# Kernel optimization log

Hardware: AMD Instinct MI355X
Metric: run time of the kernel (lower is better)

Reference implementation:

```python
import jax, jax.numpy as jnp
import numpy as np

B, T, DIM, DZ = 512, 256, 128, 256
H = 2 * DZ  # LSTM hidden size (per direction)
RESIDUAL = False


def _lstm_cell(xt, h, c, Wih, Whh, bih, bhh):
    # PyTorch gate order: input, forget, cell, output
    g = xt @ Wih.T + bih + h @ Whh.T + bhh
    i, f, gg, o = jnp.split(g, 4, axis=-1)
    c2 = jax.nn.sigmoid(f) * c + jax.nn.sigmoid(i) * jnp.tanh(gg)
    h2 = jax.nn.sigmoid(o) * jnp.tanh(c2)
    return h2, c2


def _masked_lstm(xs, lengths, Wih, Whh, bih, bhh):
    # Packed-sequence semantics: state frozen and output zero past each length.
    Bn, Tn, _ = xs.shape
    Hn = Whh.shape[1]

    def step(carry, inp):
        h, c = carry
        xt, t = inp
        h2, c2 = _lstm_cell(xt, h, c, Wih, Whh, bih, bhh)
        m = (t < lengths)[:, None]
        h = jnp.where(m, h2, h)
        c = jnp.where(m, c2, c)
        return (h, c), jnp.where(m, h2, 0.0)

    init = (jnp.zeros((Bn, Hn), xs.dtype), jnp.zeros((Bn, Hn), xs.dtype))
    _, hs = jax.lax.scan(step, init, (xs.swapaxes(0, 1), jnp.arange(Tn)))
    return hs.swapaxes(0, 1)  # [B,T,H]


def setup_inputs() -> dict:
    key = jax.random.key(0)
    ks = jax.random.split(key, 24)
    rn = lambda k, *s: jax.random.normal(k, s, jnp.float32) * 0.02
    z = jnp.zeros
    return {
        "x": jax.random.normal(ks[0], (B, T, DIM), jnp.float32),
        "x_lengths": jax.random.randint(ks[1], (B,), 1, T + 1),
        "norm_g": jnp.ones((T, DIM)), "norm_b": z((T, DIM)),
        "We": rn(ks[2], DZ, DIM), "be": z((DZ,)),
        "Wih_f": rn(ks[3], 4 * H, DZ), "Whh_f": rn(ks[4], 4 * H, H),
        "bih_f": z((4 * H,)), "bhh_f": z((4 * H,)),
        "Wih_b": rn(ks[5], 4 * H, DZ), "Whh_b": rn(ks[6], 4 * H, H),
        "bih_b": z((4 * H,)), "bhh_b": z((4 * H,)),
        "W1e": rn(ks[7], H, 2 * H), "b1e": z((H,)),
        "W2e": rn(ks[8], DZ, H), "b2e": z((DZ,)),
        "Wd": rn(ks[9], DZ, DZ), "bd": z((DZ,)),
        "Wp1": rn(ks[10], DZ, DZ), "bp1": z((DZ,)),
        "Wp2": rn(ks[11], DIM, DZ), "bp2": z((DIM,)),
        "Wih_d": rn(ks[12], 4 * H, DZ + DIM), "Whh_d": rn(ks[13], 4 * H, H),
        "bih_d": z((4 * H,)), "bhh_d": z((4 * H,)),
        "W1d": rn(ks[14], DZ, H), "b1d": z((DZ,)),
        "W2d": rn(ks[15], DIM, DZ), "b2d": z((DIM,)),
    }


def _forward(x, x_lengths, norm_g, norm_b, We, be,
             Wih_f, Whh_f, bih_f, bhh_f, Wih_b, Whh_b, bih_b, bhh_b,
             W1e, b1e, W2e, b2e,
             Wd, bd, Wp1, bp1, Wp2, bp2,
             Wih_d, Whh_d, bih_d, bhh_d, W1d, b1d, W2d, b2d):
    # ----- encoder -----
    # LayerNorm over the last two dims [T, DIM] per sample
    mu = x.mean(axis=(1, 2), keepdims=True)
    var = x.var(axis=(1, 2), keepdims=True)
    xn = (x - mu) / jnp.sqrt(var + 1e-5) * norm_g + norm_b
    xe = jax.nn.relu(xn @ We.T + be)  # [B,T,DZ]

    hs_f = _masked_lstm(xe, x_lengths, Wih_f, Whh_f, bih_f, bhh_f)
    # backward direction: reverse each valid prefix, run, scatter back
    rev_idx = jnp.clip(x_lengths[:, None] - 1 - jnp.arange(T)[None, :], 0)  # [B,T]
    xe_rev = jnp.take_along_axis(xe, rev_idx[:, :, None], axis=1)
    hs_b_rev = _masked_lstm(xe_rev, x_lengths, Wih_b, Whh_b, bih_b, bhh_b)
    hs_b = jnp.take_along_axis(hs_b_rev, rev_idx[:, :, None], axis=1)
    valid = (jnp.arange(T)[None, :] < x_lengths[:, None])[:, :, None]
    out = jnp.concatenate([hs_f, jnp.where(valid, hs_b, 0.0)], axis=-1)  # [B,T,2H]
    out = out.sum(axis=1) / x_lengths[:, None].astype(x.dtype)
    out = jax.nn.relu(out @ W1e.T + b1e)
    zlat = out @ W2e.T + b2e  # [B,DZ]

    x0 = jax.nn.relu(zlat @ Wd.T + bd)
    pose0 = jax.nn.relu(x0 @ Wp1.T + bp1) @ Wp2.T + bp2  # [B,DIM]
    h0 = jnp.zeros((x.shape[0], H), x.dtype)

    def dstep(carry, _):
        h, c, pose = carry
        inp = jnp.concatenate([x0, pose], axis=1)
        h2, c2 = _lstm_cell(inp, h, c, Wih_d, Whh_d, bih_d, bhh_d)
        h_ = jax.nn.relu(h2 @ W1d.T + b1d)
        new_pose = h_ @ W2d.T + b2d
        if RESIDUAL:
            new_pose = new_pose + pose
        return (h2, c2, new_pose), new_pose

    _, poses = jax.lax.scan(dstep, (h0, h0, pose0), None, length=T)
    return poses.swapaxes(0, 1)  # [B,T,DIM]


def reference(x, x_lengths, norm_g, norm_b, We, be,
              Wih_f, Whh_f, bih_f, bhh_f, Wih_b, Whh_b, bih_b, bhh_b,
              W1e, b1e, W2e, b2e,
              Wd, bd, Wp1, bp1, Wp2, bp2,
              Wih_d, Whh_d, bih_d, bhh_d, W1d, b1d, W2d, b2d):
    dec = _forward(x, x_lengths, norm_g, norm_b, We, be,
                   Wih_f, Whh_f, bih_f, bhh_f, Wih_b, Whh_b, bih_b, bhh_b,
                   W1e, b1e, W2e, b2e,
                   Wd, bd, Wp1, bp1, Wp2, bp2,
                   Wih_d, Whh_d, bih_d, bhh_d, W1d, b1d, W2d, b2d)
    return (x, dec, x_lengths)
```

## Files before the change

kernel.cpp:

```cpp
#include <hip/hip_runtime.h>
#include <stdint.h>
#include <math.h>

typedef unsigned short u16;
typedef unsigned char u8;
typedef unsigned u32;
typedef unsigned long long u64;
typedef short s16x8 __attribute__((ext_vector_type(8)));
typedef int i32x2 __attribute__((ext_vector_type(2)));
typedef __bf16 bv8 __attribute__((ext_vector_type(8)));
typedef float f32x4 __attribute__((ext_vector_type(4)));

#define DEV static __device__ __forceinline__

DEV float b2f(u16 x){ union{unsigned u; float f;} v; v.u=((unsigned)x)<<16; return v.f; }
DEV u16 f2b(float f){ union{float f; unsigned u;} v; v.f=f; unsigned u=v.u; u += 0x7fff + ((u>>16)&1u); return (u16)(u>>16); }
DEV float sigm(float x){ return 1.f/(1.f+__expf(-x)); }
DEV float tanh_(float x){ float cx=fminf(fmaxf(x,-20.f),20.f); float e=__expf(2.f*cx); return (e-1.f)/(e+1.f); }
DEV f32x4 mfma16(bv8 a, bv8 b, f32x4 c){ return __builtin_amdgcn_mfma_f32_16x16x32_bf16(a,b,c,0,0,0); }
DEV f32x4 mfma8(u64 a, u64 b, f32x4 c){ return __builtin_amdgcn_mfma_f32_16x16x32_fp8_fp8((long)a,(long)b,c,0,0,0); }
DEV bv8 ldf(const u16* p){ return __builtin_bit_cast(bv8, *(const s16x8*)p); }
DEV u8 f2e4(float f){ return (u8)__builtin_amdgcn_cvt_pk_fp8_f32(f, f, 0, false); }

DEV unsigned ald4(const unsigned* p){ return __hip_atomic_load(p, __ATOMIC_RELAXED, __HIP_MEMORY_SCOPE_AGENT); }

DEV void gld8(u64& d, const u8* p){
  asm volatile("global_load_dwordx2 %0, %1, off sc0 sc1" : "=&v"(d) : "v"(p));
}
DEV void gldc8(u64& d, const u8* p){
  asm volatile("global_load_dwordx2 %0, %1, off" : "=&v"(d) : "v"(p));
}
DEV void gst4(u8* p, u32 v){
  asm volatile("global_store_dword %0, %1, off sc0 sc1" :: "v"(p), "v"(v) : "memory");
}
template<int N> DEV void wvm(){
  asm volatile("s_waitcnt vmcnt(%0)" :: "i"(N) : "memory");
  __builtin_amdgcn_sched_barrier(0);
}

DEV void arrive(unsigned* flags, int my, unsigned e){
  asm volatile("s_waitcnt vmcnt(0)" ::: "memory");
  __syncthreads();
  if (threadIdx.x==0)
    __hip_atomic_store(&flags[my*32], e, __ATOMIC_RELAXED, __HIP_MEMORY_SCOPE_AGENT);
}
DEV void waitflags(unsigned* flags, int lo, int n, unsigned e){
  int t = (int)threadIdx.x;
  if (t>=lo && t<lo+n){
    unsigned v;
    do {
      asm volatile("global_load_dword %0, %1, off sc0 sc1\ns_waitcnt vmcnt(0)" : "=&v"(v) : "v"(flags + t*32) : "memory");
      if (v>=e) break;
      __builtin_amdgcn_s_sleep(1);
    } while (1);
  }
  __syncthreads();
}

struct CvtJobs { const float* s[14]; u16* d[14]; int start[14]; };

__global__ __launch_bounds__(256) void cvt_w(CvtJobs J){
  int blk = blockIdx.x, tid = threadIdx.x;
  int j = 0;
  #pragma unroll
  for (int k=1;k<14;k++) if (blk >= J.start[k]) j = k;
  size_t idx = (size_t)(blk - J.start[j])*2048 + (size_t)tid*8;
  const f32x4* ps = (const f32x4*)(J.s[j] + idx);
  f32x4 a = ps[0], b = ps[1];
  s16x8 o;
  #pragma unroll
  for (int i=0;i<4;i++){ o[i]=(short)f2b(a[i]); o[4+i]=(short)f2b(b[i]); }
  *(s16x8*)(J.d[j] + idx) = o;
}

struct Cvt8Jobs { const float* s[7]; u8* d[7]; int start[7]; };

__global__ __launch_bounds__(256) void cvt_w8(Cvt8Jobs J){
  int blk = blockIdx.x, tid = threadIdx.x;
  int j = 0;
  #pragma unroll
  for (int k=1;k<7;k++) if (blk >= J.start[k]) j = k;
  size_t idx = (size_t)(blk - J.start[j])*2048 + (size_t)tid*8;
  const f32x4* ps = (const f32x4*)(J.s[j] + idx);
  f32x4 a = ps[0], b = ps[1];
  int w0 = __builtin_amdgcn_cvt_pk_fp8_f32(a[0]*64.f, a[1]*64.f, 0, false);
  w0 = __builtin_amdgcn_cvt_pk_fp8_f32(a[2]*64.f, a[3]*64.f, w0, true);
  int w1 = __builtin_amdgcn_cvt_pk_fp8_f32(b[0]*64.f, b[1]*64.f, 0, false);
  w1 = __builtin_amdgcn_cvt_pk_fp8_f32(b[2]*64.f, b[3]*64.f, w1, true);
  i32x2 o; o[0]=w0; o[1]=w1;
  *(i32x2*)(J.d[j] + idx) = o;
}

__global__ __launch_bounds__(256) void cvt_b8(const u16* __restrict__ in, u8* __restrict__ out){
  int idx = (blockIdx.x*256 + threadIdx.x)*8;
  s16x8 v = *(const s16x8*)(in+idx);
  int w0 = __builtin_amdgcn_cvt_pk_fp8_f32(b2f((u16)v[0])*64.f, b2f((u16)v[1])*64.f, 0, false);
  w0 = __builtin_amdgcn_cvt_pk_fp8_f32(b2f((u16)v[2])*64.f, b2f((u16)v[3])*64.f, w0, true);
  int w1 = __builtin_amdgcn_cvt_pk_fp8_f32(b2f((u16)v[4])*64.f, b2f((u16)v[5])*64.f, 0, false);
  w1 = __builtin_amdgcn_cvt_pk_fp8_f32(b2f((u16)v[6])*64.f, b2f((u16)v[7])*64.f, w1, true);
  i32x2 o; o[0]=w0; o[1]=w1;
  *(i32x2*)(out + idx) = o;
}

__global__ __launch_bounds__(256) void tr_w2d(const u16* __restrict__ in, u16* __restrict__ out){
  int idx = blockIdx.x*256 + threadIdx.x;
  int r = idx>>7, p = idx&127;
  out[idx] = in[p*256 + r];
}

__global__ __launch_bounds__(256) void pb_k(const float* __restrict__ Wihd, const float* __restrict__ b2d,
                                            float* __restrict__ pb){
  int g = blockIdx.x*256 + threadIdx.x;
  const float* row = Wihd + (size_t)g*384 + 256;
  float s = 0.f;
  for (int p=0;p<128;p++) s += row[p]*b2d[p];
  pb[g] = s;
}

__global__ __launch_bounds__(256) void ln_stats(const float* __restrict__ x,
                                                float* __restrict__ mu, float* __restrict__ rstd){
  int b = blockIdx.x;
  const float* xb = x + (size_t)b*32768;
  float s1=0.f, s2=0.f;
  for (int i = threadIdx.x*4; i < 32768; i += 256*4){
    f32x4 v = *(const f32x4*)(xb+i);
    #pragma unroll
    for (int j=0;j<4;j++){ float f = v[j]; s1+=f; s2+=f*f; }
  }
  #pragma unroll
  for (int o=32;o>0;o>>=1){ s1 += __shfl_down(s1,o); s2 += __shfl_down(s2,o); }
  __shared__ float r1[4], r2[4];
  int w = threadIdx.x>>6;
  if ((threadIdx.x&63)==0){ r1[w]=s1; r2[w]=s2; }
  __syncthreads();
  if (threadIdx.x==0){
    float a=0.f,c=0.f;
    for (int i=0;i<4;i++){ a+=r1[i]; c+=r2[i]; }
    float m=a/32768.f, v=c/32768.f-m*m;
    mu[b]=m; rstd[b]=1.f/sqrtf(v+1e-5f);
  }
}

__global__ __launch_bounds__(256) void ln_gemm(const float* __restrict__ x,
    const float* __restrict__ mu, const float* __restrict__ rstd,
    const float* __restrict__ g, const float* __restrict__ bn,
    const u16* __restrict__ Wb, const float* __restrict__ be, u8* __restrict__ xe){
  __shared__ __align__(16) u16 As[128*32];
  __shared__ __align__(16) u16 Ws[128*32];
  int tid=threadIdx.x, lane=tid&63, wid=tid>>6;
  int wr=wid>>1, wc=wid&1;
  long m0=(long)blockIdx.y*128, n0=(long)blockIdx.x*128;
  int lr=lane&15, lk=(lane>>4)*8;
  f32x4 acc[4][4];
  #pragma unroll
  for (int i=0;i<4;i++)
    #pragma unroll
    for (int j=0;j<4;j++) acc[i][j]=(f32x4){0.f,0.f,0.f,0.f};

  for (int k0=0;k0<128;k0+=32){
    __syncthreads();
    #pragma unroll
    for (int c=tid;c<512;c+=256){
      int row=c>>2, kb=(c&3)*8;
      long R=m0+row;
      int b=(int)(R>>8), tt=(int)(R&255);
      float m=mu[b], rs=rstd[b];
      const f32x4* px=(const f32x4*)(x + R*128 + k0+kb);
      const f32x4* pg=(const f32x4*)(g + tt*128 + k0+kb);
      const f32x4* pb=(const f32x4*)(bn + tt*128 + k0+kb);
      f32x4 x0=px[0], x1=px[1], g0=pg[0], g1=pg[1], b0=pb[0], b1=pb[1];
      s16x8 o;
      #pragma unroll
      for (int j=0;j<4;j++){
        o[j]   = (short)f2b((x0[j]-m)*rs*g0[j] + b0[j]);
        o[4+j] = (short)f2b((x1[j]-m)*rs*g1[j] + b1[j]);
      }
      *(s16x8*)(As + row*32 + kb) = o;
    }
    #pragma unroll
    for (int c=tid;c<512;c+=256){
      int row=c>>2, kb=(c&3)*8;
      *(s16x8*)(Ws + row*32 + kb) = *(const s16x8*)(Wb + (n0+row)*128 + k0+kb);
    }
    __syncthreads();
    bv8 af[4], bf[4];
    #pragma unroll
    for (int i=0;i<4;i++) af[i] = ldf(As + (wr*64+i*16+lr)*32 + lk);
    #pragma unroll
    for (int j=0;j<4;j++) bf[j] = ldf(Ws + (wc*64+j*16+lr)*32 + lk);
    #pragma unroll
    for (int i=0;i<4;i++)
      #pragma unroll
      for (int j=0;j<4;j++) acc[i][j] = mfma16(af[i], bf[j], acc[i][j]);
  }
  #pragma unroll
  for (int i=0;i<4;i++)
    #pragma unroll
    for (int j=0;j<4;j++)
      #pragma unroll
      for (int r=0;r<4;r++){
        int m = wr*64+i*16+(lane>>4)*4+r;
        int n = wc*64+j*16+lr;
        float v = acc[i][j][r] + be[n0+n];
        xe[(m0+m)*256 + n0+n] = f2e4(fmaxf(v,0.f)*16.f);
      }
}

template<int BM, int BN, bool RELU, bool OUTF32>
__global__ __launch_bounds__(256) void gemm_bt(const u16* __restrict__ A, int lda,
                                               const u16* __restrict__ W, int ldw,
                                               const float* __restrict__ bias1, const float* __restrict__ bias2,
                                               u16* __restrict__ Cb, float* __restrict__ Cf, int ldc, int K){
  constexpr int BK=32;
  constexpr int FM=BM/32, FN=BN/32;
  __shared__ __align__(16) u16 As[BM*BK];
  __shared__ __align__(16) u16 Ws[BN*BK];
  int tid=threadIdx.x, lane=tid&63, wid=tid>>6;
  int wr=wid>>1, wc=wid&1;
  long m0=(long)blockIdx.y*BM, n0=(long)blockIdx.x*BN;
  int lr=lane&15, lk=(lane>>4)*8;
  f32x4 acc[FM][FN];
  #pragma unroll
  for (int i=0;i<FM;i++)
    #pragma unroll
    for (int j=0;j<FN;j++) acc[i][j] = (f32x4){0.f,0.f,0.f,0.f};
  for (int k0=0;k0<K;k0+=BK){
    __syncthreads();
    #pragma unroll
    for (int c=tid;c<BM*4;c+=256){
      int row=c>>2, kb=(c&3)*8;
      *(s16x8*)(As + row*BK + kb) = *(const s16x8*)(A + (m0+row)*lda + k0+kb);
    }
    #pragma unroll
    for (int c=tid;c<BN*4;c+=256){
      int row=c>>2, kb=(c&3)*8;
      *(s16x8*)(Ws + row*BK + kb) = *(const s16x8*)(W + (n0+row)*ldw + k0+kb);
    }
    __syncthreads();
    bv8 af[FM], bf[FN];
    #pragma unroll
    for (int i=0;i<FM;i++) af[i] = ldf(As + (wr*(BM/2)+i*16+lr)*BK + lk);
    #pragma unroll
    for (int j=0;j<FN;j++) bf[j] = ldf(Ws + (wc*(BN/2)+j*16+lr)*BK + lk);
    #pragma unroll
    for (int i=0;i<FM;i++)
      #pragma unroll
      for (int j=0;j<FN;j++) acc[i][j] = mfma16(af[i], bf[j], acc[i][j]);
  }
  #pragma unroll
  for (int i=0;i<FM;i++)
    #pragma unroll
    for (int j=0;j<FN;j++)
      #pragma unroll
      for (int r=0;r<4;r++){
        int m = wr*(BM/2)+i*16+(lane>>4)*4+r;
        int n = wc*(BN/2)+j*16+lr;
        float v = acc[i][j][r];
        if (bias1) v += bias1[n0+n];
        if (bias2) v += bias2[n0+n];
        if (RELU) v = fmaxf(v,0.f);
        if (OUTF32) Cf[(m0+m)*ldc + n0+n] = v;
        else        Cb[(m0+m)*ldc + n0+n] = f2b(v);
      }
}

struct EncP {
  const u8* xe; const int* lens;
  const u8 *Wihf8,*Whhf8,*Wihb8,*Whhb8;
  const float *bif,*bhf,*bib,*bhb;
  u8 *hf0,*hf1,*hb0,*hb1;
  u16* pooled;
  unsigned* flags;
};

__global__ __launch_bounds__(512,1) void enc_persist(EncP P){
  __shared__ __align__(16) u8 Wl[64*776];
  __shared__ __align__(4)  u8 Hs[128*16];
  const int tid=threadIdx.x, lane=tid&63, w=tid>>6;
  const int bx=blockIdx.x;
  const int grp=bx&7, kc=bx>>3;
  const int dir=grp>>2, bt=grp&3;
  const int lr=lane&15, q8=(lane>>4)*8;
  unsigned* flags = P.flags + grp*2048;
  const u8* Wih8 = dir? P.Wihb8 : P.Wihf8;
  const u8* Whh8 = dir? P.Whhb8 : P.Whhf8;
  const float* bi = dir? P.bib : P.bif;
  const float* bh = dir? P.bhb : P.bhf;
  u8* h0 = dir? P.hb0 : P.hf0;
  u8* h1 = dir? P.hb1 : P.hf1;

  for (int idx=tid; idx<64*96; idx+=512){
    int row=idx/96, col8=(idx%96)*8;
    int g=row>>4, c=row&15;
    size_t grow=(size_t)(g*512 + kc*16 + c);
    const u8* src = (col8<256)? (Wih8 + grow*256 + col8) : (Whh8 + grow*512 + (col8-256));
    *(u64*)(Wl + (size_t)row*776 + col8) = *(const u64*)src;
  }
  const int cg = kc*16 + lr;
  const float b_i=bi[cg]+bh[cg], b_f=bi[512+cg]+bh[512+cg];
  const float b_g=bi[1024+cg]+bh[1024+cg], b_o=bi[1536+cg]+bh[1536+cg];
  const float gsc = 1.f/1024.f;
  const int r0 = w*16 + lr;
  const int slen0 = P.lens[bt*128+r0];
  const u8* xb0 = P.xe + (size_t)(bt*128+r0)*256;
  int elen[4]; float cs[4], hh[4], asum[4];
  #pragma unroll
  for (int r=0;r<4;r++){
    int m=w*16+(lane>>4)*4+r;
    elen[r]=P.lens[bt*128+m];
    cs[r]=0.f; hh[r]=0.f; asum[r]=0.f;
  }
  __syncthreads();

  u64 rx[8];
  auto issue_rx=[&](int t_){
    int tt = dir? max(slen0-1-t_,0) : t_;
    const u8* xr = xb0 + (size_t)tt*256;
    #pragma unroll
    for (int j=0;j<8;j++) gldc8(rx[j], xr + j*32 + q8);
  };
  issue_rx(0);

  for (int t=0;t<256;t++){
    const u8* hp = (t&1)? h1 : h0;
    u8*       hn = (t&1)? h0 : h1;
    u64 fb[16];
    const u8* hr = hp + (size_t)(bt*128+r0)*512;
    waitflags(flags, 0, 16, (unsigned)t);
    #pragma unroll
    for (int j=0;j<8;j++) gld8(fb[j], hr + j*32 + q8);
    waitflags(flags, 16, 16, (unsigned)t);
    #pragma unroll
    for (int j=8;j<16;j++) gld8(fb[j], hr + j*32 + q8);
    f32x4 acc[4];
    #pragma unroll
    for (int g=0;g<4;g++) acc[g]=(f32x4){0.f,0.f,0.f,0.f};
    wvm<16>();
    #pragma unroll
    for (int j=0;j<8;j++){
      u64 a = rx[j];
      #pragma unroll
      for (int g=0;g<4;g++){
        u64 b = *(const u64*)(Wl + (size_t)(g*16+lr)*776 + j*32 + q8);
        acc[g]=mfma8(a,b,acc[g]);
      }
    }
    wvm<8>();
    #pragma unroll
    for (int j=0;j<8;j++){
      u64 a = fb[j];
      #pragma unroll
      for (int g=0;g<4;g++){
        u64 b = *(const u64*)(Wl + (size_t)(g*16+lr)*776 + 256 + j*32 + q8);
        acc[g]=mfma8(a,b,acc[g]);
      }
    }
    wvm<0>();
    #pragma unroll
    for (int j=8;j<16;j++){
      u64 a = fb[j];
      #pragma unroll
      for (int g=0;g<4;g++){
        u64 b = *(const u64*)(Wl + (size_t)(g*16+lr)*776 + 256 + j*32 + q8);
        acc[g]=mfma8(a,b,acc[g]);
      }
    }
    #pragma unroll
    for (int r=0;r<4;r++){
      int m=w*16+(lane>>4)*4+r;
      if (t<elen[r]){
        float iv=sigm(acc[0][r]*gsc+b_i), fv=sigm(acc[1][r]*gsc+b_f);
        float gv=tanh_(acc[2][r]*gsc+b_g), ov=sigm(acc[3][r]*gsc+b_o);
        float c2=fv*cs[r]+iv*gv, h2v=ov*tanh_(c2);
        cs[r]=c2; hh[r]=h2v; asum[r]+=h2v;
      }
      Hs[m*16+lr]=f2e4(hh[r]*16.f);
    }
    __syncthreads();
    {
      int sm=tid>>2, pt=tid&3;
      gst4(hn + (size_t)(bt*128+sm)*512 + kc*16 + pt*4, *(const u32*)(Hs + sm*16 + pt*4));
    }
    arrive(flags, kc, (unsigned)(t+1));
    if (t<255) issue_rx(t+1);
  }
  #pragma unroll
  for (int r=0;r<4;r++){
    int m=w*16+(lane>>4)*4+r;
    P.pooled[(size_t)(bt*128+m)*1024 + (size_t)dir*512 + cg]=f2b(asum[r]/(float)elen[r]);
  }
}

struct DecP {
  const u8 *Whhd8, *Wcmp8, *W1d8, *W2d8;
  const float *gix, *gp0, *pb, *b1d, *b2d;
  u8 *h0,*h1,*r1a,*r1b;
  float* outd;
  unsigned* flags;
};

__global__ __launch_bounds__(256,1) void dec_persist(DecP P){
  __shared__ __align__(8) u8 Wh [64*520];
  __shared__ __align__(8) u8 Wc [64*264];
  __shared__ __align__(8) u8 F12[16*520];
  __shared__ __align__(4) u8 Hs[64*16];
  const int tid=threadIdx.x, lane=tid&63, w=tid>>6;
  const int bx=blockIdx.x;
  const int grp=bx&7, kc=bx>>3;
  const int g0 = grp*64;
  const int lr=lane&15, q8=(lane>>4)*8;
  unsigned* flags = P.flags + grp*2048;

  for (int idx=tid; idx<64*64; idx+=256){
    int row=idx>>6, col8=(idx&63)*8;
    int g=row>>4, c=row&15;
    size_t grow=(size_t)(g*512+kc*16+c);
    *(u64*)(Wh + (size_t)row*520 + col8) = *(const u64*)(P.Whhd8 + grow*512 + col8);
  }
  for (int idx=tid; idx<64*32; idx+=256){
    int row=idx>>5, col8=(idx&31)*8;
    int g=row>>4, c=row&15;
    size_t grow=(size_t)(g*512+kc*16+c);
    *(u64*)(Wc + (size_t)row*264 + col8) = *(const u64*)(P.Wcmp8 + grow*256 + col8);
  }
  if (kc<16){
    for (int idx=tid; idx<16*64; idx+=256){
      int rr=idx>>6, col8=(idx&63)*8;
      *(u64*)(F12 + (size_t)rr*520 + col8) = *(const u64*)(P.W1d8 + (size_t)(kc*16+rr)*512 + col8);
    }
  } else if (kc<24){
    for (int idx=tid; idx<16*32; idx+=256){
      int rr=idx>>5, col8=(idx&31)*8;
      *(u64*)(F12 + (size_t)rr*264 + col8) = *(const u64*)(P.W2d8 + (size_t)((kc-16)*16+rr)*256 + col8);
    }
  }
  float gx[4][4]; float pbr[4];
  #pragma unroll
  for (int g=0;g<4;g++)
    #pragma unroll
    for (int r=0;r<4;r++){
      int m=w*16+(lane>>4)*4+r;
      gx[g][r]=P.gix[(size_t)(g0+m)*2048 + (size_t)g*512 + kc*16 + lr];
    }
  #pragma unroll
  for (int g=0;g<4;g++) pbr[g] = P.pb[(size_t)g*512 + kc*16 + lr];
  const float b1=(kc<16)? P.b1d[kc*16+lr] : 0.f;
  const float b2=(kc>=16&&kc<24)? P.b2d[(kc-16)*16+lr] : 0.f;
  const float gsc = 1.f/1024.f;
  const int ar = w*16 + lr;
  float cs[4];
  f32x4 gh[4];
  #pragma unroll
  for (int r=0;r<4;r++) cs[r]=0.f;
  #pragma unroll
  for (int g=0;g<4;g++) gh[g]=(f32x4){0.f,0.f,0.f,0.f};
  __syncthreads();

  for (int t=0;t<256;t++){
    const u8* r1rd = (t&1)? P.r1b : P.r1a;
    u8* hn = (t&1)? P.h0 : P.h1;
    f32x4 acc[4]; float ascale;
    if (t==0){
      ascale = 1.f;
      #pragma unroll
      for (int g=0;g<4;g++)
        #pragma unroll
        for (int r=0;r<4;r++){
          int m=w*16+(lane>>4)*4+r;
          acc[g][r] = gx[g][r] + P.gp0[(size_t)(g0+m)*2048 + (size_t)g*512 + kc*16 + lr];
        }
    } else {
      ascale = gsc;
      const u8* rb = r1rd + (size_t)(g0+ar)*256;
      u64 fb[8];
      waitflags(flags, 32, 8, (unsigned)t);
      #pragma unroll
      for (int j=0;j<4;j++) gld8(fb[j], rb + j*32 + q8);
      waitflags(flags, 40, 8, (unsigned)t);
      #pragma unroll
      for (int j=4;j<8;j++) gld8(fb[j], rb + j*32 + q8);
      #pragma unroll
      for (int g=0;g<4;g++)
        acc[g] = gh[g] + (f32x4){(gx[g][0]+pbr[g])*1024.f,(gx[g][1]+pbr[g])*1024.f,
                                 (gx[g][2]+pbr[g])*1024.f,(gx[g][3]+pbr[g])*1024.f};
      wvm<4>();
      #pragma unroll
      for (int j=0;j<4;j++){
        u64 a=fb[j];
        #pragma unroll
        for (int g=0;g<4;g++){
          u64 b = *(const u64*)(Wc + (size_t)(g*16+lr)*264 + j*32 + q8);
          acc[g]=mfma8(a,b,acc[g]);
        }
      }
      wvm<0>();
      #pragma unroll
      for (int j=4;j<8;j++){
        u64 a=fb[j];
        #pragma unroll
        for (int g=0;g<4;g++){
          u64 b = *(const u64*)(Wc + (size_t)(g*16+lr)*264 + j*32 + q8);
          acc[g]=mfma8(a,b,acc[g]);
        }
      }
    }
    #pragma unroll
    for (int r=0;r<4;r++){
      float iv=sigm(acc[0][r]*ascale), fv=sigm(acc[1][r]*ascale);
      float gv=tanh_(acc[2][r]*ascale), ov=sigm(acc[3][r]*ascale);
      float c2=fv*cs[r]+iv*gv, h2v=ov*tanh_(c2);
      cs[r]=c2;
      int m=w*16+(lane>>4)*4+r;
      Hs[m*16+lr]=f2e4(h2v*16.f);
    }
    __syncthreads();
    {
      int sm=tid>>2, pt=tid&3;
      gst4(hn + (size_t)(g0+sm)*512 + kc*16 + pt*4, *(const u32*)(Hs + sm*16 + pt*4));
    }
    arrive(flags, kc, (unsigned)(t+1));
    if (kc>=16 && kc<24 && t>0){
      const u8* rb = r1rd + (size_t)(g0+ar)*256;
      f32x4 fa2=(f32x4){0.f,0.f,0.f,0.f};
      u64 fb[8];
      #pragma unroll
      for (int j=0;j<8;j++) gld8(fb[j], rb + j*32 + q8);
      wvm<0>();
      #pragma unroll
      for (int j=0;j<8;j++){
        u64 b = *(const u64*)(F12 + (size_t)lr*264 + j*32 + q8);
        fa2=mfma8(fb[j],b,fa2);
      }
      int pc=(kc-16)*16+lr;
      #pragma unroll
      for (int r=0;r<4;r++){
        int m=w*16+(lane>>4)*4+r;
        __builtin_nontemporal_store(fa2[r]*gsc+b2, P.outd + (size_t)(g0+m)*32768 + (size_t)(t-1)*128 + pc);
      }
    }
    u64 hbf[16];
    const u8* hb = hn + (size_t)(g0+ar)*512;
    waitflags(flags, 0, 16, (unsigned)(t+1));
    #pragma unroll
    for (int j=0;j<8;j++) gld8(hbf[j], hb + j*32 + q8);
    waitflags(flags, 16, 16, (unsigned)(t+1));
    #pragma unroll
    for (int j=8;j<16;j++) gld8(hbf[j], hb + j*32 + q8);
    f32x4 gn[4]; f32x4 fa=(f32x4){0.f,0.f,0.f,0.f};
    #pragma unroll
    for (int g=0;g<4;g++) gn[g]=(f32x4){0.f,0.f,0.f,0.f};
    wvm<8>();
    #pragma unroll
    for (int j=0;j<8;j++){
      u64 a=hbf[j];
      #pragma unroll
      for (int g=0;g<4;g++){
        u64 b = *(const u64*)(Wh + (size_t)(g*16+lr)*520 + j*32 + q8);
        gn[g]=mfma8(a,b,gn[g]);
      }
      if (kc<16){
        u64 b = *(const u64*)(F12 + (size_t)lr*520 + j*32 + q8);
        fa=mfma8(a,b,fa);
      }
    }
    wvm<0>();
    #pragma unroll
    for (int j=8;j<16;j++){
      u64 a=hbf[j];
      #pragma unroll
      for (int g=0;g<4;g++){
        u64 b = *(const u64*)(Wh + (size_t)(g*16+lr)*520 + j*32 + q8);
        gn[g]=mfma8(a,b,gn[g]);
      }
      if (kc<16){
        u64 b = *(const u64*)(F12 + (size_t)lr*520 + j*32 + q8);
        fa=mfma8(a,b,fa);
      }
    }
    #pragma unroll
    for (int g=0;g<4;g++) gh[g]=gn[g];
    if (kc<16){
      u8* r1w = (t&1)? P.r1a : P.r1b;
      #pragma unroll
      for (int r=0;r<4;r++){
        int m=w*16+(lane>>4)*4+r;
        Hs[m*16+lr]=f2e4(fmaxf(fa[r]*gsc+b1,0.f)*16.f);
      }
      __syncthreads();
      {
        int sm=tid>>2, pt=tid&3;
        gst4(r1w + (size_t)(g0+sm)*256 + kc*16 + pt*4, *(const u32*)(Hs + sm*16 + pt*4));
      }
      arrive(flags, 32+kc, (unsigned)(t+1));
    }
  }
  if (kc>=16 && kc<24){
    waitflags(flags, 32, 16, 256u);
    const u8* rb = P.r1a + (size_t)(g0+ar)*256;
    f32x4 fa2=(f32x4){0.f,0.f,0.f,0.f};
    u64 fb[8];
    #pragma unroll
    for (int j=0;j<8;j++) gld8(fb[j], rb + j*32 + q8);
    wvm<0>();
    #pragma unroll
    for (int j=0;j<8;j++){
      u64 b = *(const u64*)(F12 + (size_t)lr*264 + j*32 + q8);
      fa2=mfma8(fb[j],b,fa2);
    }
    int pc=(kc-16)*16+lr;
    #pragma unroll
    for (int r=0;r<4;r++){
      int m=w*16+(lane>>4)*4+r;
      __builtin_nontemporal_store(fa2[r]*gsc+b2, P.outd + (size_t)(g0+m)*32768 + (size_t)255*128 + pc);
    }
  }
}

__global__ __launch_bounds__(512) void len_cast(const int* __restrict__ lens, float* __restrict__ out){
  int i = threadIdx.x;
  if (i < 512) out[i] = (float)lens[i];
}

extern "C" void kernel_launch(void* const* d_in, const int* in_sizes, int n_in,
                              void* d_out, int out_size, void* d_ws, size_t ws_size,
                              hipStream_t stream){
  (void)in_sizes; (void)n_in; (void)out_size; (void)ws_size;
  const float* x      = (const float*)d_in[0];
  const int*   lens   = (const int*)d_in[1];
  const float* ng     = (const float*)d_in[2];
  const float* nb     = (const float*)d_in[3];
  const float* We     = (const float*)d_in[4];
  const float* be     = (const float*)d_in[5];
  const float* Wih_f  = (const float*)d_in[6];
  const float* Whh_f  = (const float*)d_in[7];
  const float* bih_f  = (const float*)d_in[8];
  const float* bhh_f  = (const float*)d_in[9];
  const float* Wih_b  = (const float*)d_in[10];
  const float* Whh_b  = (const float*)d_in[11];
  const float* bih_b  = (const float*)d_in[12];
  const float* bhh_b  = (const float*)d_in[13];
  const float* W1e    = (const float*)d_in[14];
  const float* b1e    = (const float*)d_in[15];
  const float* W2e    = (const float*)d_in[16];
  const float* b2e    = (const float*)d_in[17];
  const float* Wd     = (const float*)d_in[18];
  const float* bd     = (const float*)d_in[19];
  const float* Wp1    = (const float*)d_in[20];
  const float* bp1    = (const float*)d_in[21];
  const float* Wp2    = (const float*)d_in[22];
  const float* bp2    = (const float*)d_in[23];
  const float* Wih_d  = (const float*)d_in[24];
  const float* Whh_d  = (const float*)d_in[25];
  const float* bih_d  = (const float*)d_in[26];
  const float* bhh_d  = (const float*)d_in[27];
  const float* W1d    = (const float*)d_in[28];
  const float* b1d    = (const float*)d_in[29];
  const float* W2d    = (const float*)d_in[30];
  const float* b2d    = (const float*)d_in[31];

  char* p = (char*)d_ws;
  auto carve = [&](size_t bytes)->void*{ void* r=(void*)p; p += (bytes+255)&~(size_t)255; return r; };
  float* mu   = (float*)carve(512*4);
  float* rstd = (float*)carve(512*4);
  u8* xe8     = (u8*)carve((size_t)33554432);
  u16* wWe  = (u16*)carve(32768*2);
  u16* wIhf = (u16*)carve(524288*2);
  u16* wHhf = (u16*)carve(1048576*2);
  u16* wIhb = (u16*)carve(524288*2);
  u16* wHhb = (u16*)carve(1048576*2);
  u16* wW1e = (u16*)carve(524288*2);
  u16* wW2e = (u16*)carve(131072*2);
  u16* wWd  = (u16*)carve(65536*2);
  u16* wWp1 = (u16*)carve(65536*2);
  u16* wWp2 = (u16*)carve(32768*2);
  u16* wIhd = (u16*)carve(786432*2);
  u16* wHhd = (u16*)carve(1048576*2);
  u16* wW1d = (u16*)carve(131072*2);
  u16* wW2d = (u16*)carve(32768*2);
  u16* wW2dT  = (u16*)carve(32768*2);
  u16* wWcomp = (u16*)carve(524288*2);
  u8* wIhf8 = (u8*)carve(524288);
  u8* wHhf8 = (u8*)carve(1048576);
  u8* wIhb8 = (u8*)carve(524288);
  u8* wHhb8 = (u8*)carve(1048576);
  u8* wHhd8 = (u8*)carve(1048576);
  u8* wW1d8 = (u8*)carve(131072);
  u8* wW2d8 = (u8*)carve(32768);
  u8* wWcmp8= (u8*)carve(524288);
  float* pbv  = (float*)carve(2048*4);
  float* gp0f = (float*)carve((size_t)1048576*4);
  u8* hf0  = (u8*)carve(262144);
  u8* hf1  = (u8*)carve(262144);
  u8* hb0  = (u8*)carve(262144);
  u8* hb1  = (u8*)carve(262144);
  u8* hd0  = (u8*)carve(262144);
  u8* hd1  = (u8*)carve(262144);
  u8* r1a8 = (u8*)carve(131072);
  u8* r1b8 = (u8*)carve(131072);
  u16* pooled = (u16*)carve(1048576);
  u16* out1   = (u16*)carve(524288);
  u16* zlat   = (u16*)carve(262144);
  u16* x0     = (u16*)carve(262144);
  u16* t0     = (u16*)carve(262144);
  float* gix  = (float*)carve(4194304);
  u16* pose   = (u16*)carve(131072);
  unsigned* barflags = (unsigned*)carve(16*2048*4);

  float* out_x   = (float*)d_out;
  float* out_dec = out_x + 16777216;
  float* out_len = out_x + 33554432;

  hipMemcpyAsync(out_x, x, (size_t)16777216*4, hipMemcpyDeviceToDevice, stream);
  hipMemsetAsync(hf0,0,262144,stream);
  hipMemsetAsync(hb0,0,262144,stream);
  hipMemsetAsync(hd0,0,262144,stream);
  hipMemsetAsync(barflags,0,16*2048*4,stream);

  CvtJobs J;
  const float* srcs[14] = {We,Wih_f,Whh_f,Wih_b,Whh_b,W1e,W2e,Wd,Wp1,Wp2,Wih_d,Whh_d,W1d,W2d};
  u16* dsts[14] = {wWe,wIhf,wHhf,wIhb,wHhb,wW1e,wW2e,wWd,wWp1,wWp2,wIhd,wHhd,wW1d,wW2d};
  int ns[14] = {32768,524288,1048576,524288,1048576,524288,131072,65536,65536,32768,786432,1048576,131072,32768};
  int blk=0;
  for (int i=0;i<14;i++){ J.s[i]=srcs[i]; J.d[i]=dsts[i]; J.start[i]=blk; blk += ns[i]/2048; }
  cvt_w<<<blk,256,0,stream>>>(J);

  Cvt8Jobs J8;
  const float* s8[7] = {Wih_f,Whh_f,Wih_b,Whh_b,Whh_d,W1d,W2d};
  u8* d8[7] = {wIhf8,wHhf8,wIhb8,wHhb8,wHhd8,wW1d8,wW2d8};
  int n8[7] = {524288,1048576,524288,1048576,1048576,131072,32768};
  int blk8=0;
  for (int i=0;i<7;i++){ J8.s[i]=s8[i]; J8.d[i]=d8[i]; J8.start[i]=blk8; blk8 += n8[i]/2048; }
  cvt_w8<<<blk8,256,0,stream>>>(J8);

  tr_w2d<<<128,256,0,stream>>>(wW2d, wW2dT);
  pb_k<<<8,256,0,stream>>>(Wih_d, b2d, pbv);
  gemm_bt<64,64,false,false><<<dim3(4,32),256,0,stream>>>(wIhd+256,384, wW2dT,128, nullptr,nullptr, wWcomp,nullptr,256,128);
  cvt_b8<<<256,256,0,stream>>>(wWcomp, wWcmp8);

  ln_stats<<<512,256,0,stream>>>(x,mu,rstd);
  ln_gemm<<<dim3(2,1024),256,0,stream>>>(x,mu,rstd,ng,nb,wWe,be,xe8);

  EncP EP = {xe8,lens,wIhf8,wHhf8,wIhb8,wHhb8,bih_f,bhh_f,bih_b,bhh_b,hf0,hf1,hb0,hb1,pooled,barflags};
  {
    void* ea[] = {&EP};
    if (hipLaunchCooperativeKernel((void*)enc_persist, dim3(256), dim3(512), ea, 0, stream) != hipSuccess)
      enc_persist<<<256,512,0,stream>>>(EP);
  }

  gemm_bt<64,64,true ,false><<<dim3(8,8),256,0,stream>>>(pooled,1024,wW1e,1024,b1e,nullptr,out1,nullptr,512,1024);
  gemm_bt<64,64,false,false><<<dim3(4,8),256,0,stream>>>(out1,512,wW2e,512,b2e,nullptr,zlat,nullptr,256,512);
  gemm_bt<64,64,true ,false><<<dim3(4,8),256,0,stream>>>(zlat,256,wWd,256,bd,nullptr,x0,nullptr,256,256);
  gemm_bt<64,64,true ,false><<<dim3(4,8),256,0,stream>>>(x0,256,wWp1,256,bp1,nullptr,t0,nullptr,256,256);
  gemm_bt<64,64,false,false><<<dim3(2,8),256,0,stream>>>(t0,256,wWp2,256,bp2,nullptr,pose,nullptr,128,256);
  gemm_bt<64,128,false,true><<<dim3(16,8),256,0,stream>>>(x0,256,wIhd,384,bih_d,bhh_d,nullptr,gix,2048,256);
  gemm_bt<64,128,false,true><<<dim3(16,8),256,0,stream>>>(pose,128,wIhd+256,384,nullptr,nullptr,nullptr,gp0f,2048,128);

  DecP DP = {wHhd8,wWcmp8,wW1d8,wW2d8, gix,gp0f,pbv,b1d,b2d, hd0,hd1,r1a8,r1b8, out_dec, barflags + 8*2048};
  {
    void* da[] = {&DP};
    if (hipLaunchCooperativeKernel((void*)dec_persist, dim3(256), dim3(256), da, 0, stream) != hipSuccess)
      dec_persist<<<256,256,0,stream>>>(DP);
  }

  len_cast<<<1,512,0,stream>>>(lens,out_len);
}
```

Measured before the change: 4.088 ms.

## Recompute decoder relu hidden layer redundantly per block to drop second grid barrier

Result: slower. 8.192 ms (+100.4%).

```diff
diff --git a/kernel.cpp b/kernel.cpp
--- a/kernel.cpp
+++ b/kernel.cpp
@@ -394,7 +394,7 @@
 struct DecP {
   const u8 *Whhd8, *Wcmp8, *W1d8, *W2d8;
   const float *gix, *gp0, *pb, *b1d, *b2d;
-  u8 *h0,*h1,*r1a,*r1b;
+  u8 *h0,*h1;
   float* outd;
   unsigned* flags;
 };
@@ -402,7 +402,9 @@
 __global__ __launch_bounds__(256,1) void dec_persist(DecP P){
   __shared__ __align__(8) u8 Wh [64*520];
   __shared__ __align__(8) u8 Wc [64*264];
-  __shared__ __align__(8) u8 F12[16*520];
+  __shared__ __align__(8) u8 F2s[16*264];
+  __shared__ __align__(8) u8 h8 [64*520];
+  __shared__ __align__(8) u8 r1s[64*264];
   __shared__ __align__(4) u8 Hs[64*16];
   const int tid=threadIdx.x, lane=tid&63, w=tid>>6;
   const int bx=blockIdx.x;
@@ -423,18 +425,13 @@
     size_t grow=(size_t)(g*512+kc*16+c);
     *(u64*)(Wc + (size_t)row*264 + col8) = *(const u64*)(P.Wcmp8 + grow*256 + col8);
   }
-  if (kc<16){
-    for (int idx=tid; idx<16*64; idx+=256){
-      int rr=idx>>6, col8=(idx&63)*8;
-      *(u64*)(F12 + (size_t)rr*520 + col8) = *(const u64*)(P.W1d8 + (size_t)(kc*16+rr)*512 + col8);
-    }
-  } else if (kc<24){
+  if (kc>=16 && kc<24){
     for (int idx=tid; idx<16*32; idx+=256){
       int rr=idx>>5, col8=(idx&31)*8;
-      *(u64*)(F12 + (size_t)rr*264 + col8) = *(const u64*)(P.W2d8 + (size_t)((kc-16)*16+rr)*256 + col8);
-    }
-  }
-  float gx[4][4]; float pbr[4];
+      *(u64*)(F2s + (size_t)rr*264 + col8) = *(const u64*)(P.W2d8 + (size_t)((kc-16)*16+rr)*256 + col8);
+    }
+  }
+  float gx[4][4]; float pbr[4]; float b1v[4];
   #pragma unroll
   for (int g=0;g<4;g++)
     #pragma unroll
@@ -444,21 +441,73 @@
     }
   #pragma unroll
   for (int g=0;g<4;g++) pbr[g] = P.pb[(size_t)g*512 + kc*16 + lr];
-  const float b1=(kc<16)? P.b1d[kc*16+lr] : 0.f;
+  #pragma unroll
+  for (int n2=0;n2<4;n2++) b1v[n2] = P.b1d[w*64 + n2*16 + lr];
   const float b2=(kc>=16&&kc<24)? P.b2d[(kc-16)*16+lr] : 0.f;
   const float gsc = 1.f/1024.f;
-  const int ar = w*16 + lr;
+  const int r0 = w*16 + lr;
   float cs[4];
-  f32x4 gh[4];
   #pragma unroll
   for (int r=0;r<4;r++) cs[r]=0.f;
-  #pragma unroll
-  for (int g=0;g<4;g++) gh[g]=(f32x4){0.f,0.f,0.f,0.f};
   __syncthreads();
 
+  auto r1phase=[&](const u8* hp, f32x4* accg ){
+    u64 fb[16];
+    const u8* hr = hp + (size_t)(g0+r0)*512;
+    #pragma unroll
+    for (int j=0;j<16;j++) gld8(fb[j], hr + j*32 + q8);
+    wvm<0>();
+    #pragma unroll
+    for (int j=0;j<16;j++) *(u64*)(h8 + (size_t)r0*520 + j*32 + q8) = fb[j];
+    __syncthreads();
+    f32x4 racc[4][4];
+    #pragma unroll
+    for (int mi=0;mi<4;mi++)
+      #pragma unroll
+      for (int n2=0;n2<4;n2++) racc[mi][n2]=(f32x4){0.f,0.f,0.f,0.f};
+    u64 wb0[4], wb1[4];
+    auto issueW=[&](u64* wb, int kk){
+      #pragma unroll
+      for (int n2=0;n2<4;n2++)
+        gldc8(wb[n2], P.W1d8 + (size_t)(w*64+n2*16+lr)*512 + kk*32 + q8);
+    };
+    issueW(wb0,0); issueW(wb1,1);
+    #pragma unroll
+    for (int kk=0;kk<16;kk++){
+      if (kk<15) wvm<4>(); else wvm<0>();
+      u64* wb = (kk&1)? wb1 : wb0;
+      u64 a[4];
+      #pragma unroll
+      for (int mi=0;mi<4;mi++) a[mi] = *(const u64*)(h8 + (size_t)(mi*16+lr)*520 + kk*32 + q8);
+      #pragma unroll
+      for (int n2=0;n2<4;n2++)
+        #pragma unroll
+        for (int mi=0;mi<4;mi++) racc[mi][n2]=mfma8(a[mi], wb[n2], racc[mi][n2]);
+      if (accg){
+        #pragma unroll
+        for (int g=0;g<4;g++){
+          u64 b = *(const u64*)(Wh + (size_t)(g*16+lr)*520 + kk*32 + q8);
+          accg[g]=mfma8(a[w], b, accg[g]);
+        }
+      }
+      if (kk<14) issueW((kk&1)? wb1 : wb0, kk+2);
+    }
+    #pragma unroll
+    for (int mi=0;mi<4;mi++)
+      #pragma unroll
+      for (int n2=0;n2<4;n2++)
+        #pragma unroll
+        for (int r=0;r<4;r++){
+          int sm = mi*16 + (lane>>4)*4 + r;
+          int cn = w*64 + n2*16 + lr;
+          r1s[(size_t)sm*264 + cn] = f2e4(fmaxf(racc[mi][n2][r]*gsc + b1v[n2], 0.f)*16.f);
+        }
+    __syncthreads();
+  };
+
   for (int t=0;t<256;t++){
-    const u8* r1rd = (t&1)? P.r1b : P.r1a;
-    u8* hn = (t&1)? P.h0 : P.h1;
+    const u8* hp = (t&1)? P.h1 : P.h0;
+    u8*       hn = (t&1)? P.h0 : P.h1;
     f32x4 acc[4]; float ascale;
     if (t==0){
       ascale = 1.f;
@@ -471,36 +520,19 @@
         }
     } else {
       ascale = gsc;
-      const u8* rb = r1rd + (size_t)(g0+ar)*256;
-      u64 fb[8];
-      waitflags(flags, 32, 8, (unsigned)t);
-      #pragma unroll
-      for (int j=0;j<4;j++) gld8(fb[j], rb + j*32 + q8);
-      waitflags(flags, 40, 8, (unsigned)t);
-      #pragma unroll
-      for (int j=4;j<8;j++) gld8(fb[j], rb + j*32 + q8);
+      waitflags(flags, 0, 32, (unsigned)t);
       #pragma unroll
       for (int g=0;g<4;g++)
-        acc[g] = gh[g] + (f32x4){(gx[g][0]+pbr[g])*1024.f,(gx[g][1]+pbr[g])*1024.f,
-                                 (gx[g][2]+pbr[g])*1024.f,(gx[g][3]+pbr[g])*1024.f};
-      wvm<4>();
-      #pragma unroll
-      for (int j=0;j<4;j++){
-        u64 a=fb[j];
+        acc[g] = (f32x4){(gx[g][0]+pbr[g])*1024.f,(gx[g][1]+pbr[g])*1024.f,
+                         (gx[g][2]+pbr[g])*1024.f,(gx[g][3]+pbr[g])*1024.f};
+      r1phase(hp, acc);
+      #pragma unroll
+      for (int kk=0;kk<8;kk++){
+        u64 a2 = *(const u64*)(r1s + (size_t)r0*264 + kk*32 + q8);
         #pragma unroll
         for (int g=0;g<4;g++){
-          u64 b = *(const u64*)(Wc + (size_t)(g*16+lr)*264 + j*32 + q8);
-          acc[g]=mfma8(a,b,acc[g]);
-        }
-      }
-      wvm<0>();
-      #pragma unroll
-      for (int j=4;j<8;j++){
-        u64 a=fb[j];
-        #pragma unroll
-        for (int g=0;g<4;g++){
-          u64 b = *(const u64*)(Wc + (size_t)(g*16+lr)*264 + j*32 + q8);
-          acc[g]=mfma8(a,b,acc[g]);
+          u64 b = *(const u64*)(Wc + (size_t)(g*16+lr)*264 + kk*32 + q8);
+          acc[g]=mfma8(a2,b,acc[g]);
         }
       }
     }
@@ -520,16 +552,12 @@
     }
     arrive(flags, kc, (unsigned)(t+1));
     if (kc>=16 && kc<24 && t>0){
-      const u8* rb = r1rd + (size_t)(g0+ar)*256;
       f32x4 fa2=(f32x4){0.f,0.f,0.f,0.f};
-      u64 fb[8];
-      #pragma unroll
-      for (int j=0;j<8;j++) gld8(fb[j], rb + j*32 + q8);
-      wvm<0>();
-      #pragma unroll
-      for (int j=0;j<8;j++){
-        u64 b = *(const u64*)(F12 + (size_t)lr*264 + j*32 + q8);
-        fa2=mfma8(fb[j],b,fa2);
+      #pragma unroll
+      for (int kk=0;kk<8;kk++){
+        u64 a2 = *(const u64*)(r1s + (size_t)r0*264 + kk*32 + q8);
+        u64 b  = *(const u64*)(F2s + (size_t)lr*264 + kk*32 + q8);
+        fa2=mfma8(a2,b,fa2);
       }
       int pc=(kc-16)*16+lr;
       #pragma unroll
@@ -538,74 +566,16 @@
         __builtin_nontemporal_store(fa2[r]*gsc+b2, P.outd + (size_t)(g0+m)*32768 + (size_t)(t-1)*128 + pc);
       }
     }
-    u64 hbf[16];
-    const u8* hb = hn + (size_t)(g0+ar)*512;
-    waitflags(flags, 0, 16, (unsigned)(t+1));
-    #pragma unroll
-    for (int j=0;j<8;j++) gld8(hbf[j], hb + j*32 + q8);
-    waitflags(flags, 16, 16, (unsigned)(t+1));
-    #pragma unroll
-    for (int j=8;j<16;j++) gld8(hbf[j], hb + j*32 + q8);
-    f32x4 gn[4]; f32x4 fa=(f32x4){0.f,0.f,0.f,0.f};
-    #pragma unroll
-    for (int g=0;g<4;g++) gn[g]=(f32x4){0.f,0.f,0.f,0.f};
-    wvm<8>();
-    #pragma unroll
-    for (int j=0;j<8;j++){
-      u64 a=hbf[j];
-      #pragma unroll
-      for (int g=0;g<4;g++){
-        u64 b = *(const u64*)(Wh + (size_t)(g*16+lr)*520 + j*32 + q8);
-        gn[g]=mfma8(a,b,gn[g]);
-      }
-      if (kc<16){
-        u64 b = *(const u64*)(F12 + (size_t)lr*520 + j*32 + q8);
-        fa=mfma8(a,b,fa);
-      }
-    }
-    wvm<0>();
-    #pragma unroll
-    for (int j=8;j<16;j++){
-      u64 a=hbf[j];
-      #pragma unroll
-      for (int g=0;g<4;g++){
-        u64 b = *(const u64*)(Wh + (size_t)(g*16+lr)*520 + j*32 + q8);
-        gn[g]=mfma8(a,b,gn[g]);
-      }
-      if (kc<16){
-        u64 b = *(const u64*)(F12 + (size_t)lr*520 + j*32 + q8);
-        fa=mfma8(a,b,fa);
-      }
-    }
-    #pragma unroll
-    for (int g=0;g<4;g++) gh[g]=gn[g];
-    if (kc<16){
-      u8* r1w = (t&1)? P.r1a : P.r1b;
-      #pragma unroll
-      for (int r=0;r<4;r++){
-        int m=w*16+(lane>>4)*4+r;
-        Hs[m*16+lr]=f2e4(fmaxf(fa[r]*gsc+b1,0.f)*16.f);
-      }
-      __syncthreads();
-      {
-        int sm=tid>>2, pt=tid&3;
-        gst4(r1w + (size_t)(g0+sm)*256 + kc*16 + pt*4, *(const u32*)(Hs + sm*16 + pt*4));
-      }
-      arrive(flags, 32+kc, (unsigned)(t+1));
-    }
   }
   if (kc>=16 && kc<24){
-    waitflags(flags, 32, 16, 256u);
-    const u8* rb = P.r1a + (size_t)(g0+ar)*256;
+    waitflags(flags, 0, 32, 256u);
+    r1phase(P.h0, nullptr);
     f32x4 fa2=(f32x4){0.f,0.f,0.f,0.f};
-    u64 fb[8];
-    #pragma unroll
-    for (int j=0;j<8;j++) gld8(fb[j], rb + j*32 + q8);
-    wvm<0>();
-    #pragma unroll
-    for (int j=0;j<8;j++){
-      u64 b = *(const u64*)(F12 + (size_t)lr*264 + j*32 + q8);
-      fa2=mfma8(fb[j],b,fa2);
+    #pragma unroll
+    for (int kk=0;kk<8;kk++){
+      u64 a2 = *(const u64*)(r1s + (size_t)r0*264 + kk*32 + q8);
+      u64 b  = *(const u64*)(F2s + (size_t)lr*264 + kk*32 + q8);
+      fa2=mfma8(a2,b,fa2);
     }
     int pc=(kc-16)*16+lr;
     #pragma unroll
@@ -695,8 +665,6 @@
   u8* hb1  = (u8*)carve(262144);
   u8* hd0  = (u8*)carve(262144);
   u8* hd1  = (u8*)carve(262144);
-  u8* r1a8 = (u8*)carve(131072);
-  u8* r1b8 = (u8*)carve(131072);
   u16* pooled = (u16*)carve(1048576);
   u16* out1   = (u16*)carve(524288);
   u16* zlat   = (u16*)carve(262144);
@@ -755,7 +723,7 @@
   gemm_bt<64,128,false,true><<<dim3(16,8),256,0,stream>>>(x0,256,wIhd,384,bih_d,bhh_d,nullptr,gix,2048,256);
   gemm_bt<64,128,false,true><<<dim3(16,8),256,0,stream>>>(pose,128,wIhd+256,384,nullptr,nullptr,nullptr,gp0f,2048,128);
 
-  DecP DP = {wHhd8,wWcmp8,wW1d8,wW2d8, gix,gp0f,pbv,b1d,b2d, hd0,hd1,r1a8,r1b8, out_dec, barflags + 8*2048};
+  DecP DP = {wHhd8,wWcmp8,wW1d8,wW2d8, gix,gp0f,pbv,b1d,b2d, hd0,hd1, out_dec, barflags + 8*2048};
   {
     void* da[] = {&DP};
     if (hipLaunchCooperativeKernel((void*)dec_persist, dim3(256), dim3(256), da, 0, stream) != hipSuccess)
```
